# Kernel tuning notes

Hardware: AMD Instinct MI355X
Metric: run time of the kernel (lower is better)

Reference implementation:

```python
import jax, jax.numpy as jnp
import numpy as np


def setup_inputs() -> dict:
    key = jax.random.key(0)
    ip = jax.random.normal(key, (8, 256, 128, 128), dtype=jnp.float32)
    return {"ip": ip}


def reference(ip):
    b, C, H, W = ip.shape
    two_c = 2 * C
    # precomputed complex shift grid: exp(-1j*2*pi*(C-0.5)*v/(2C)), v = 0..2C-1
    v = jnp.arange(two_c, dtype=jnp.float32)
    angle = -2.0 * jnp.pi * (C - 0.5) * v / two_c
    shift = (jnp.cos(angle) + 1j * jnp.sin(angle)).astype(jnp.complex64)  # [2C]

    viDct = ip * two_c                                   # [b, C, H, W]
    flip_neg = -viDct[:, 1:][:, ::-1]                    # [b, C-1, H, W]
    zeros = jnp.zeros((b, 1, H, W), dtype=ip.dtype)
    rev = jnp.concatenate([viDct, zeros, flip_neg], axis=1)  # [b, 2C, H, W]
    rev = rev.astype(jnp.complex64) * shift[None, :, None, None]
    vxx = jnp.fft.ifft(rev, axis=1)                      # norm='backward' (default)
    out = vxx[:, :C][:, ::-1].real                       # first C, flipped, real part
    return out.astype(ip.dtype)
```

## Files before the change

### kernel.cpp

```cpp
#include <hip/hip_runtime.h>
#include <math.h>

#define NB   8
#define NC   256
#define NHW  (128 * 128)

#define BM 128
#define BN 64
#define BK 32
#define NITER (NC / BK)

typedef __attribute__((ext_vector_type(4))) float f32x4;
typedef __attribute__((ext_vector_type(8))) short bf16x8;

__device__ __forceinline__ unsigned short f2bf(float f) {
    unsigned u = __builtin_bit_cast(unsigned, f);
    u += 0x7fffu + ((u >> 16) & 1u);
    return (unsigned short)(u >> 16);
}

__device__ __forceinline__ unsigned pack2bf(float a, float b) {
    unsigned lo = __builtin_bit_cast(unsigned, a);
    lo += 0x7fffu + ((lo >> 16) & 1u);
    unsigned hi = __builtin_bit_cast(unsigned, b);
    hi += 0x7fffu + ((hi >> 16) & 1u);
    return (lo >> 16) | (hi & 0xffff0000u);
}

__global__ void coef_kernel(unsigned short* __restrict__ coef) {
    int idx = blockIdx.x * 256 + threadIdx.x;
    int c = idx >> 8;
    int k = idx & 255;
    int t = (k * (2 * c + 1)) & 1023;
    float v = (k == 0) ? 1.0f : 2.0f * cosf((float)t * (float)(M_PI / 512.0));
    coef[idx] = f2bf(v);
}

__device__ __forceinline__ void gload_lds16(const void* g, void* l) {
    __builtin_amdgcn_global_load_lds(
        (const __attribute__((address_space(1))) unsigned int*)g,
        (__attribute__((address_space(3))) unsigned int*)l,
        16, 0, 0);
}


__global__ __launch_bounds__(256, 4)
void dct_gemm(const float* __restrict__ X, const unsigned short* __restrict__ Mcoef,
              float* __restrict__ Out) {
    __shared__ __align__(16) unsigned char lds[24576];

    const int tid  = threadIdx.x;
    const int lane = tid & 63;
    const int wave = tid >> 6;
    const int m16  = lane & 15;
    const int quad = lane >> 4;
    const int wm   = wave >> 1;
    const int wn   = wave & 1;

    const int p0 = blockIdx.x * BN;
    const int c0 = blockIdx.y * BM;
    const size_t bbase = (size_t)blockIdx.z * (NC * NHW);
    const float* Xg = X + bbase;
    float* Og = Out + bbase;

    const int bA0 = wave * 2048 + lane * 16;
    const int bA1 = bA0 + 1024;
    const int rA0 = bA0 >> 6, rA1 = bA1 >> 6;
    const int qA0 = ((bA0 >> 4) & 3) ^ ((rA0 >> 1) & 3);
    const int qA1 = ((bA1 >> 4) & 3) ^ ((rA1 >> 1) & 3);
    const unsigned short* aSrc0 = Mcoef + (c0 + rA0) * NC + qA0 * 8;
    const unsigned short* aSrc1 = Mcoef + (c0 + rA1) * NC + qA1 * 8;

    const int sp = lane;
    const float* xSrc = Xg + (size_t)(wave * 8) * NHW + p0 + sp;
    const int xWoff = sp * 64 + ((wave ^ ((sp >> 1) & 3)) << 4);

    int offA[4], offB[2];
#pragma unroll
    for (int mt = 0; mt < 4; mt++) {
        int r = wm * 64 + mt * 16 + m16;
        offA[mt] = r * 64 + ((quad ^ ((r >> 1) & 3)) << 4);
    }
#pragma unroll
    for (int nt = 0; nt < 2; nt++) {
        int r = wn * 32 + nt * 16 + m16;
        offB[nt] = r * 64 + ((quad ^ ((r >> 1) & 3)) << 4);
    }

    f32x4 acc[4][2];
#pragma unroll
    for (int i = 0; i < 4; i++)
#pragma unroll
        for (int j = 0; j < 2; j++) acc[i][j] = (f32x4){0.f, 0.f, 0.f, 0.f};

    {
        float xv[8];
#pragma unroll
        for (int j = 0; j < 8; j++) xv[j] = xSrc[(size_t)j * NHW];
        gload_lds16(aSrc0, lds + 0 + bA0);
        gload_lds16(aSrc1, lds + 0 + bA1);
        int4 w = { (int)pack2bf(xv[0], xv[1]), (int)pack2bf(xv[2], xv[3]),
                   (int)pack2bf(xv[4], xv[5]), (int)pack2bf(xv[6], xv[7]) };
        *(int4*)(lds + 16384 + xWoff) = w;
    }
    __syncthreads();

#pragma unroll
    for (int t = 0; t < NITER; t++) {
        const int cb = t & 1;
        const unsigned char* Ac = lds + (cb ? 8192 : 0);
        const unsigned char* Xc = lds + 16384 + (cb ? 4096 : 0);
        unsigned char* As = lds + (cb ? 0 : 8192);
        unsigned char* Xs = lds + 16384 + (cb ? 0 : 4096);

        float xv[8];
        if (t + 1 < NITER) {
            const int k0 = (t + 1) * BK;
#pragma unroll
            for (int j = 0; j < 8; j++) xv[j] = xSrc[(size_t)(k0 + j) * NHW];
            gload_lds16(aSrc0 + k0, As + bA0);
            gload_lds16(aSrc1 + k0, As + bA1);
        }

        bf16x8 af[4], bfr[2];
#pragma unroll
        for (int mt = 0; mt < 4; mt++) af[mt] = *(const bf16x8*)(Ac + offA[mt]);
#pragma unroll
        for (int nt = 0; nt < 2; nt++) bfr[nt] = *(const bf16x8*)(Xc + offB[nt]);
#pragma unroll
        for (int mt = 0; mt < 4; mt++)
#pragma unroll
            for (int nt = 0; nt < 2; nt++)
                acc[mt][nt] = __builtin_amdgcn_mfma_f32_16x16x32_bf16(
                    af[mt], bfr[nt], acc[mt][nt], 0, 0, 0);

        if (t + 1 < NITER) {
            int4 w = { (int)pack2bf(xv[0], xv[1]), (int)pack2bf(xv[2], xv[3]),
                       (int)pack2bf(xv[4], xv[5]), (int)pack2bf(xv[6], xv[7]) };
            *(int4*)(Xs + xWoff) = w;
            __syncthreads();
        }
    }

#pragma unroll
    for (int mt = 0; mt < 4; mt++) {
        const int cc = c0 + wm * 64 + mt * 16 + quad * 4;
#pragma unroll
        for (int nt = 0; nt < 2; nt++) {
            const int pp = p0 + wn * 32 + nt * 16 + m16;
            float* o = Og + (size_t)cc * NHW + pp;
#pragma unroll
            for (int r = 0; r < 4; r++)
                __builtin_nontemporal_store(acc[mt][nt][r], o + (size_t)r * NHW);
        }
    }
}

extern "C" void kernel_launch(void* const* d_in, const int* in_sizes, int n_in,
                              void* d_out, int out_size, void* d_ws, size_t ws_size,
                              hipStream_t stream) {
    const float* ip = (const float*)d_in[0];
    float* out = (float*)d_out;
    unsigned short* coef = (unsigned short*)d_ws;

    coef_kernel<<<dim3(256), dim3(256), 0, stream>>>(coef);

    dim3 grid(NHW / BN, NC / BM, NB);
    dct_gemm<<<grid, dim3(256), 0, stream>>>(ip, coef, out);
}
```

Baseline: 259.6 us.

## Cover all channels per block so each input tile is read once

Raises the M tile to the full 256 channels and BK to 64, using 512-thread blocks and an 80KB LDS double buffer with an 8-way XOR swizzle. The grid's channel dimension collapses to 1, so every input pixel column is loaded and converted to bf16 once instead of once per channel half, cutting global read traffic on this memory-bound GEMM. The output stores also switch from nontemporal to ordinary stores. In exchange, the large LDS footprint and bigger blocks lower the number of resident blocks per CU, which can weaken latency hiding.

Result: faster. 235.2 us (-9.4%).

```diff
diff --git a/kernel.cpp b/kernel.cpp
--- a/kernel.cpp
+++ b/kernel.cpp
@@ -5,10 +5,12 @@
 #define NC   256
 #define NHW  (128 * 128)
 
-#define BM 128
+#define BM 256
 #define BN 64
-#define BK 32
+#define BK 64
 #define NITER (NC / BK)
+
+#define XBASE 65536
 
 typedef __attribute__((ext_vector_type(4))) float f32x4;
 typedef __attribute__((ext_vector_type(8))) short bf16x8;
@@ -44,10 +46,10 @@
 }
 
 
-__global__ __launch_bounds__(256, 4)
+__global__ __launch_bounds__(512, 4)
 void dct_gemm(const float* __restrict__ X, const unsigned short* __restrict__ Mcoef,
               float* __restrict__ Out) {
-    __shared__ __align__(16) unsigned char lds[24576];
+    __shared__ __align__(16) unsigned char lds[81920];
 
     const int tid  = threadIdx.x;
     const int lane = tid & 63;
@@ -58,33 +60,33 @@
     const int wn   = wave & 1;
 
     const int p0 = blockIdx.x * BN;
-    const int c0 = blockIdx.y * BM;
     const size_t bbase = (size_t)blockIdx.z * (NC * NHW);
     const float* Xg = X + bbase;
     float* Og = Out + bbase;
 
-    const int bA0 = wave * 2048 + lane * 16;
-    const int bA1 = bA0 + 1024;
-    const int rA0 = bA0 >> 6, rA1 = bA1 >> 6;
-    const int qA0 = ((bA0 >> 4) & 3) ^ ((rA0 >> 1) & 3);
-    const int qA1 = ((bA1 >> 4) & 3) ^ ((rA1 >> 1) & 3);
-    const unsigned short* aSrc0 = Mcoef + (c0 + rA0) * NC + qA0 * 8;
-    const unsigned short* aSrc1 = Mcoef + (c0 + rA1) * NC + qA1 * 8;
+    const int trow = tid >> 3;
+    const int tj   = (tid & 7) ^ (trow & 7);
+    const unsigned short* aS = Mcoef + trow * NC + tj * 8;
+    const int aDst = tid * 16;
 
-    const int sp = lane;
+    const int sp = tid & 63;
     const float* xSrc = Xg + (size_t)(wave * 8) * NHW + p0 + sp;
-    const int xWoff = sp * 64 + ((wave ^ ((sp >> 1) & 3)) << 4);
+    const int xWoff = sp * 128 + ((wave ^ (sp & 7)) << 4);
 
-    int offA[4], offB[2];
+    int offA[4][2], offB[2][2];
 #pragma unroll
     for (int mt = 0; mt < 4; mt++) {
-        int r = wm * 64 + mt * 16 + m16;
-        offA[mt] = r * 64 + ((quad ^ ((r >> 1) & 3)) << 4);
+        const int r = wm * 64 + mt * 16 + m16;
+#pragma unroll
+        for (int kk = 0; kk < 2; kk++)
+            offA[mt][kk] = (r << 7) + (((kk * 4 + quad) ^ (m16 & 7)) << 4);
     }
 #pragma unroll
     for (int nt = 0; nt < 2; nt++) {
-        int r = wn * 32 + nt * 16 + m16;
-        offB[nt] = r * 64 + ((quad ^ ((r >> 1) & 3)) << 4);
+        const int r = wn * 32 + nt * 16 + m16;
+#pragma unroll
+        for (int kk = 0; kk < 2; kk++)
+            offB[nt][kk] = XBASE + (r << 7) + (((kk * 4 + quad) ^ (m16 & 7)) << 4);
     }
 
     f32x4 acc[4][2];
@@ -97,42 +99,47 @@
         float xv[8];
 #pragma unroll
         for (int j = 0; j < 8; j++) xv[j] = xSrc[(size_t)j * NHW];
-        gload_lds16(aSrc0, lds + 0 + bA0);
-        gload_lds16(aSrc1, lds + 0 + bA1);
+#pragma unroll
+        for (int i = 0; i < 4; i++)
+            gload_lds16(aS + i * 64 * NC, lds + i * 8192 + aDst);
         int4 w = { (int)pack2bf(xv[0], xv[1]), (int)pack2bf(xv[2], xv[3]),
                    (int)pack2bf(xv[4], xv[5]), (int)pack2bf(xv[6], xv[7]) };
-        *(int4*)(lds + 16384 + xWoff) = w;
+        *(int4*)(lds + XBASE + xWoff) = w;
     }
     __syncthreads();
 
 #pragma unroll
     for (int t = 0; t < NITER; t++) {
         const int cb = t & 1;
-        const unsigned char* Ac = lds + (cb ? 8192 : 0);
-        const unsigned char* Xc = lds + 16384 + (cb ? 4096 : 0);
-        unsigned char* As = lds + (cb ? 0 : 8192);
-        unsigned char* Xs = lds + 16384 + (cb ? 0 : 4096);
+        const unsigned char* Ac = lds + cb * 32768;
+        const unsigned char* Xc = lds + cb * 8192;
+        unsigned char* As = lds + (cb ^ 1) * 32768;
+        unsigned char* Xs = lds + XBASE + (cb ^ 1) * 8192;
 
         float xv[8];
         if (t + 1 < NITER) {
             const int k0 = (t + 1) * BK;
 #pragma unroll
             for (int j = 0; j < 8; j++) xv[j] = xSrc[(size_t)(k0 + j) * NHW];
-            gload_lds16(aSrc0 + k0, As + bA0);
-            gload_lds16(aSrc1 + k0, As + bA1);
+#pragma unroll
+            for (int i = 0; i < 4; i++)
+                gload_lds16(aS + i * 64 * NC + k0, As + i * 8192 + aDst);
         }
 
-        bf16x8 af[4], bfr[2];
 #pragma unroll
-        for (int mt = 0; mt < 4; mt++) af[mt] = *(const bf16x8*)(Ac + offA[mt]);
+        for (int kk = 0; kk < 2; kk++) {
+            bf16x8 af[4], bfr[2];
 #pragma unroll
-        for (int nt = 0; nt < 2; nt++) bfr[nt] = *(const bf16x8*)(Xc + offB[nt]);
+            for (int mt = 0; mt < 4; mt++) af[mt] = *(const bf16x8*)(Ac + offA[mt][kk]);
 #pragma unroll
-        for (int mt = 0; mt < 4; mt++)
+            for (int nt = 0; nt < 2; nt++) bfr[nt] = *(const bf16x8*)(Xc + offB[nt][kk]);
 #pragma unroll
-            for (int nt = 0; nt < 2; nt++)
-                acc[mt][nt] = __builtin_amdgcn_mfma_f32_16x16x32_bf16(
-                    af[mt], bfr[nt], acc[mt][nt], 0, 0, 0);
+            for (int mt = 0; mt < 4; mt++)
+#pragma unroll
+                for (int nt = 0; nt < 2; nt++)
+                    acc[mt][nt] = __builtin_amdgcn_mfma_f32_16x16x32_bf16(
+                        af[mt], bfr[nt], acc[mt][nt], 0, 0, 0);
+        }
 
         if (t + 1 < NITER) {
             int4 w = { (int)pack2bf(xv[0], xv[1]), (int)pack2bf(xv[2], xv[3]),
@@ -144,14 +151,14 @@
 
 #pragma unroll
     for (int mt = 0; mt < 4; mt++) {
-        const int cc = c0 + wm * 64 + mt * 16 + quad * 4;
+        const int cc = wm * 64 + mt * 16 + quad * 4;
 #pragma unroll
         for (int nt = 0; nt < 2; nt++) {
             const int pp = p0 + wn * 32 + nt * 16 + m16;
             float* o = Og + (size_t)cc * NHW + pp;
 #pragma unroll
             for (int r = 0; r < 4; r++)
-                __builtin_nontemporal_store(acc[mt][nt][r], o + (size_t)r * NHW);
+                o[(size_t)r * NHW] = acc[mt][nt][r];
         }
     }
 }
@@ -165,6 +172,6 @@
 
     coef_kernel<<<dim3(256), dim3(256), 0, stream>>>(coef);
 
-    dim3 grid(NHW / BN, NC / BM, NB);
-    dct_gemm<<<grid, dim3(256), 0, stream>>>(ip, coef, out);
+    dim3 grid(NHW / BN, 1, NB);
+    dct_gemm<<<grid, dim3(512), 0, stream>>>(ip, coef, out);
 }
```

## Exploit DCT coefficient symmetry and keep half coefficient matrix resident in LDS

Applied to the files above, without the earlier changes.

Computes only the first 128 rows of the cosine coefficient matrix. It derives the mirrored output rows (255-c) by flipping the sign of odd-k inputs, which halves the coefficient data and the coefficient-generation work. The kernel becomes persistent-style: 512 blocks of 512 threads each load the 128x256 bf16 coefficients into LDS once, then loop over 4 spatial tiles with the full K=256 resident and double-buffered input tiles. This removes the repeated coefficient reloads and the per-K-step syncs, at the cost of a large LDS footprint (128KB) that limits occupancy. It also switches to regular (temporal) stores.

New measurement: 243.9 us. 6.1% less time.

```diff
diff --git a/kernel.cpp b/kernel.cpp
--- a/kernel.cpp
+++ b/kernel.cpp
@@ -5,13 +5,12 @@
 #define NC   256
 #define NHW  (128 * 128)
 
-#define BM 128
-#define BN 64
-#define BK 32
-#define NITER (NC / BK)
+#define TILES 4
+#define XB 65536
 
 typedef __attribute__((ext_vector_type(4))) float f32x4;
 typedef __attribute__((ext_vector_type(8))) short bf16x8;
+typedef __attribute__((ext_vector_type(4))) unsigned int u32x4;
 
 __device__ __forceinline__ unsigned short f2bf(float f) {
     unsigned u = __builtin_bit_cast(unsigned, f);
@@ -25,6 +24,12 @@
     unsigned hi = __builtin_bit_cast(unsigned, b);
     hi += 0x7fffu + ((hi >> 16) & 1u);
     return (lo >> 16) | (hi & 0xffff0000u);
+}
+
+__device__ __forceinline__ bf16x8 flip_odd(bf16x8 b) {
+    u32x4 u = __builtin_bit_cast(u32x4, b);
+    u ^= (u32x4){0x80000000u, 0x80000000u, 0x80000000u, 0x80000000u};
+    return __builtin_bit_cast(bf16x8, u);
 }
 
 __global__ void coef_kernel(unsigned short* __restrict__ coef) {
@@ -44,10 +49,10 @@
 }
 
 
-__global__ __launch_bounds__(256, 4)
+__global__ __launch_bounds__(512, 2)
 void dct_gemm(const float* __restrict__ X, const unsigned short* __restrict__ Mcoef,
               float* __restrict__ Out) {
-    __shared__ __align__(16) unsigned char lds[24576];
+    __shared__ __align__(16) unsigned char lds[131072];
 
     const int tid  = threadIdx.x;
     const int lane = tid & 63;
@@ -57,102 +62,101 @@
     const int wm   = wave >> 1;
     const int wn   = wave & 1;
 
-    const int p0 = blockIdx.x * BN;
-    const int c0 = blockIdx.y * BM;
-    const size_t bbase = (size_t)blockIdx.z * (NC * NHW);
-    const float* Xg = X + bbase;
-    float* Og = Out + bbase;
-
-    const int bA0 = wave * 2048 + lane * 16;
-    const int bA1 = bA0 + 1024;
-    const int rA0 = bA0 >> 6, rA1 = bA1 >> 6;
-    const int qA0 = ((bA0 >> 4) & 3) ^ ((rA0 >> 1) & 3);
-    const int qA1 = ((bA1 >> 4) & 3) ^ ((rA1 >> 1) & 3);
-    const unsigned short* aSrc0 = Mcoef + (c0 + rA0) * NC + qA0 * 8;
-    const unsigned short* aSrc1 = Mcoef + (c0 + rA1) * NC + qA1 * 8;
-
-    const int sp = lane;
-    const float* xSrc = Xg + (size_t)(wave * 8) * NHW + p0 + sp;
-    const int xWoff = sp * 64 + ((wave ^ ((sp >> 1) & 3)) << 4);
-
-    int offA[4], offB[2];
 #pragma unroll
-    for (int mt = 0; mt < 4; mt++) {
-        int r = wm * 64 + mt * 16 + m16;
-        offA[mt] = r * 64 + ((quad ^ ((r >> 1) & 3)) << 4);
-    }
-#pragma unroll
-    for (int nt = 0; nt < 2; nt++) {
-        int r = wn * 32 + nt * 16 + m16;
-        offB[nt] = r * 64 + ((quad ^ ((r >> 1) & 3)) << 4);
+    for (int i = 0; i < 8; i++) {
+        const int L = i * 8192 + tid * 16;
+        const int row = L >> 9;
+        const int sl = ((L >> 4) & 31) ^ (row & 15);
+        gload_lds16(Mcoef + row * 256 + sl * 8, lds + L);
     }
 
-    f32x4 acc[4][2];
-#pragma unroll
-    for (int i = 0; i < 4; i++)
-#pragma unroll
-        for (int j = 0; j < 2; j++) acc[i][j] = (f32x4){0.f, 0.f, 0.f, 0.f};
+    const int sp  = tid & 63;
+    const int skb = wave * 32;
+
+    const int g0 = blockIdx.x * TILES;
 
     {
-        float xv[8];
+        const float* s = X + (size_t)(g0 >> 8) * (NC * NHW) + (size_t)skb * NHW + (g0 & 255) * 64 + sp;
+        float v[32];
 #pragma unroll
-        for (int j = 0; j < 8; j++) xv[j] = xSrc[(size_t)j * NHW];
-        gload_lds16(aSrc0, lds + 0 + bA0);
-        gload_lds16(aSrc1, lds + 0 + bA1);
-        int4 w = { (int)pack2bf(xv[0], xv[1]), (int)pack2bf(xv[2], xv[3]),
-                   (int)pack2bf(xv[4], xv[5]), (int)pack2bf(xv[6], xv[7]) };
-        *(int4*)(lds + 16384 + xWoff) = w;
+        for (int j = 0; j < 32; j++) v[j] = s[(size_t)j * NHW];
+#pragma unroll
+        for (int w = 0; w < 4; w++) {
+            int4 q = { (int)pack2bf(v[8*w+0], v[8*w+1]), (int)pack2bf(v[8*w+2], v[8*w+3]),
+                       (int)pack2bf(v[8*w+4], v[8*w+5]), (int)pack2bf(v[8*w+6], v[8*w+7]) };
+            *(int4*)(lds + XB + sp * 512 + (((wave * 4 + w) ^ (sp & 15)) << 4)) = q;
+        }
     }
     __syncthreads();
 
+    const int aB0 = (wm * 32 + m16) * 512;
+    const int xB0 = (wn * 32 + m16) * 512;
+
+    for (int t = 0; t < TILES; t++) {
+        const int g = g0 + t;
+        const unsigned char* Xc = lds + XB + (t & 1) * 32768;
+        unsigned char* Xs = lds + XB + ((t + 1) & 1) * 32768;
+
+        float v[32];
+        if (t + 1 < TILES) {
+            const int g1 = g + 1;
+            const float* s = X + (size_t)(g1 >> 8) * (NC * NHW) + (size_t)skb * NHW + (g1 & 255) * 64 + sp;
 #pragma unroll
-    for (int t = 0; t < NITER; t++) {
-        const int cb = t & 1;
-        const unsigned char* Ac = lds + (cb ? 8192 : 0);
-        const unsigned char* Xc = lds + 16384 + (cb ? 4096 : 0);
-        unsigned char* As = lds + (cb ? 0 : 8192);
-        unsigned char* Xs = lds + 16384 + (cb ? 0 : 4096);
-
-        float xv[8];
-        if (t + 1 < NITER) {
-            const int k0 = (t + 1) * BK;
-#pragma unroll
-            for (int j = 0; j < 8; j++) xv[j] = xSrc[(size_t)(k0 + j) * NHW];
-            gload_lds16(aSrc0 + k0, As + bA0);
-            gload_lds16(aSrc1 + k0, As + bA1);
+            for (int j = 0; j < 32; j++) v[j] = s[(size_t)j * NHW];
         }
 
-        bf16x8 af[4], bfr[2];
+        f32x4 acc[2][2][2];
 #pragma unroll
-        for (int mt = 0; mt < 4; mt++) af[mt] = *(const bf16x8*)(Ac + offA[mt]);
+        for (int a = 0; a < 2; a++)
 #pragma unroll
-        for (int nt = 0; nt < 2; nt++) bfr[nt] = *(const bf16x8*)(Xc + offB[nt]);
+            for (int b = 0; b < 2; b++)
 #pragma unroll
-        for (int mt = 0; mt < 4; mt++)
-#pragma unroll
-            for (int nt = 0; nt < 2; nt++)
-                acc[mt][nt] = __builtin_amdgcn_mfma_f32_16x16x32_bf16(
-                    af[mt], bfr[nt], acc[mt][nt], 0, 0, 0);
-
-        if (t + 1 < NITER) {
-            int4 w = { (int)pack2bf(xv[0], xv[1]), (int)pack2bf(xv[2], xv[3]),
-                       (int)pack2bf(xv[4], xv[5]), (int)pack2bf(xv[6], xv[7]) };
-            *(int4*)(Xs + xWoff) = w;
-            __syncthreads();
-        }
-    }
+                for (int h = 0; h < 2; h++) acc[a][b][h] = (f32x4){0.f, 0.f, 0.f, 0.f};
 
 #pragma unroll
-    for (int mt = 0; mt < 4; mt++) {
-        const int cc = c0 + wm * 64 + mt * 16 + quad * 4;
+        for (int kk = 0; kk < 8; kk++) {
+            const int so = (((kk * 4 + quad) ^ m16) << 4);
+            bf16x8 af0 = *(const bf16x8*)(lds + aB0 + so);
+            bf16x8 af1 = *(const bf16x8*)(lds + aB0 + 16 * 512 + so);
+            bf16x8 bf0 = *(const bf16x8*)(Xc + xB0 + so);
+            bf16x8 bf1 = *(const bf16x8*)(Xc + xB0 + 16 * 512 + so);
+            bf16x8 bn0 = flip_odd(bf0);
+            bf16x8 bn1 = flip_odd(bf1);
+            acc[0][0][0] = __builtin_amdgcn_mfma_f32_16x16x32_bf16(af0, bf0, acc[0][0][0], 0, 0, 0);
+            acc[0][1][0] = __builtin_amdgcn_mfma_f32_16x16x32_bf16(af0, bf1, acc[0][1][0], 0, 0, 0);
+            acc[1][0][0] = __builtin_amdgcn_mfma_f32_16x16x32_bf16(af1, bf0, acc[1][0][0], 0, 0, 0);
+            acc[1][1][0] = __builtin_amdgcn_mfma_f32_16x16x32_bf16(af1, bf1, acc[1][1][0], 0, 0, 0);
+            acc[0][0][1] = __builtin_amdgcn_mfma_f32_16x16x32_bf16(af0, bn0, acc[0][0][1], 0, 0, 0);
+            acc[0][1][1] = __builtin_amdgcn_mfma_f32_16x16x32_bf16(af0, bn1, acc[0][1][1], 0, 0, 0);
+            acc[1][0][1] = __builtin_amdgcn_mfma_f32_16x16x32_bf16(af1, bn0, acc[1][0][1], 0, 0, 0);
+            acc[1][1][1] = __builtin_amdgcn_mfma_f32_16x16x32_bf16(af1, bn1, acc[1][1][1], 0, 0, 0);
+        }
+
+        if (t + 1 < TILES) {
 #pragma unroll
-        for (int nt = 0; nt < 2; nt++) {
-            const int pp = p0 + wn * 32 + nt * 16 + m16;
-            float* o = Og + (size_t)cc * NHW + pp;
+            for (int w = 0; w < 4; w++) {
+                int4 q = { (int)pack2bf(v[8*w+0], v[8*w+1]), (int)pack2bf(v[8*w+2], v[8*w+3]),
+                           (int)pack2bf(v[8*w+4], v[8*w+5]), (int)pack2bf(v[8*w+6], v[8*w+7]) };
+                *(int4*)(Xs + sp * 512 + (((wave * 4 + w) ^ (sp & 15)) << 4)) = q;
+            }
+        }
+
+        float* Ob = Out + (size_t)(g >> 8) * (NC * NHW) + (g & 255) * 64;
 #pragma unroll
-            for (int r = 0; r < 4; r++)
-                __builtin_nontemporal_store(acc[mt][nt][r], o + (size_t)r * NHW);
+        for (int mt = 0; mt < 2; mt++) {
+            const int cL = wm * 32 + mt * 16 + quad * 4;
+#pragma unroll
+            for (int nt = 0; nt < 2; nt++) {
+                const int pp = wn * 32 + nt * 16 + m16;
+#pragma unroll
+                for (int r = 0; r < 4; r++) {
+                    Ob[(size_t)(cL + r) * NHW + pp]       = acc[mt][nt][0][r];
+                    Ob[(size_t)(255 - cL - r) * NHW + pp] = acc[mt][nt][1][r];
+                }
+            }
         }
+
+        if (t + 1 < TILES) __syncthreads();
     }
 }
 
@@ -163,8 +167,7 @@
     float* out = (float*)d_out;
     unsigned short* coef = (unsigned short*)d_ws;
 
-    coef_kernel<<<dim3(256), dim3(256), 0, stream>>>(coef);
+    coef_kernel<<<dim3(128), dim3(256), 0, stream>>>(coef);
 
-    dim3 grid(NHW / BN, NC / BM, NB);
-    dct_gemm<<<grid, dim3(256), 0, stream>>>(ip, coef, out);
+    dct_gemm<<<dim3(512), dim3(512), 0, stream>>>(ip, coef, out);
 }
```
